# Kernel optimization log

Measured on AMD Instinct MI355X. Metric: run time of the kernel, lower is better.

## Reference

```python
import jax, jax.numpy as jnp
import numpy as np

B, N, C, DIM, K, E, NB = 16, 20000, 64, 128, 3, 640000, 3


def setup_inputs() -> dict:
    key = jax.random.key(0)
    ks = jax.random.split(key, 8)
    x = jax.random.normal(ks[0], (B, N * C), jnp.float32)
    edge_index = jax.random.randint(ks[1], (2, E), 0, N, jnp.int32)
    edge_weight = jax.random.uniform(ks[2], (E,), jnp.float32)
    # ChebConv: K Linear(C, dim, bias=False) weights + one shared bias per conv
    cheb_w = jax.random.normal(ks[3], (NB, K, C, DIM), jnp.float32) / np.float32(np.sqrt(C))
    cheb_b = jnp.zeros((NB, DIM), jnp.float32)
    beta = jnp.full((NB,), 0.5, jnp.float32)  # Swish beta, one shared act per block
    w1 = jax.random.normal(ks[4], (NB, DIM, DIM), jnp.float32) / np.float32(np.sqrt(DIM))
    b1 = jnp.zeros((NB, DIM), jnp.float32)
    w2 = jax.random.normal(ks[5], (NB, DIM, C), jnp.float32) / np.float32(np.sqrt(DIM))
    b2 = jnp.zeros((NB, C), jnp.float32)
    return dict(x=x, edge_index=edge_index, edge_weight=edge_weight,
                cheb_w=cheb_w, cheb_b=cheb_b, beta=beta, w1=w1, b1=b1, w2=w2, b2=b2)


def swish(x, beta):
    # (x * sigmoid(x * softplus(beta))) / 1.1
    return x * jax.nn.sigmoid(x * jax.nn.softplus(beta)) / 1.1


def reference(x, edge_index, edge_weight, cheb_w, cheb_b, beta, w1, b1, w2, b2):
    src, dst = edge_index[0], edge_index[1]
    # PyG ChebConv norm with lambda_max=2, sym: Lhat = L - I = -D^{-1/2} A D^{-1/2}
    deg = jax.ops.segment_sum(edge_weight, src, num_segments=N)
    dinv = jnp.where(deg > 0, jax.lax.rsqrt(jnp.maximum(deg, 1e-12)), 0.0)
    w = -dinv[src] * edge_weight * dinv[dst]  # [E]

    def spmm(h):  # h: [B, N, F] -> Lhat @ h per batch
        msg = h[:, src, :] * w[None, :, None]          # gather + scale, [B, E, F]
        return jnp.zeros_like(h).at[:, dst, :].add(msg)  # scatter-add

    h = x.reshape(B, N, C)
    for b in range(NB):  # fixed small layer loop
        # Chebyshev recurrence
        t0 = h
        t1 = spmm(t0)
        out = jnp.einsum('bnc,cd->bnd', t0, cheb_w[b, 0]) \
            + jnp.einsum('bnc,cd->bnd', t1, cheb_w[b, 1])
        tm2, tm1 = t0, t1
        for k in range(2, K):
            tk = 2.0 * spmm(tm1) - tm2
            out = out + jnp.einsum('bnc,cd->bnd', tk, cheb_w[b, k])
            tm2, tm1 = tm1, tk
        out = out + cheb_b[b]
        g = swish(out, beta[b])
        g = swish(g @ w1[b] + b1[b], beta[b])
        Fx = g @ w2[b] + b2[b]
        h = h + Fx  # invertible residual: output = Fx + x
    return h.reshape(B, N * C)
```

## Files before the change

### kernel.cpp

```cpp
#include <hip/hip_runtime.h>

namespace {
constexpr int   B_   = 16;
constexpr int   N_   = 20000;
constexpr int   C_   = 64;
constexpr int   DIM_ = 128;
constexpr int   E_   = 640000;
constexpr int   NB_  = 3;
constexpr int   ROW_ = B_ * C_;
constexpr int   NR_  = N_ * B_;

constexpr int   LDP  = 200;

constexpr int   PH_   = 16;
constexpr int   PCOL_ = ROW_ / PH_;
constexpr int   NPB_  = 16;
constexpr int   NCHK_ = N_ / NPB_;
constexpr int   NBIN_ = 1024;
constexpr int   NXCD_ = 8;
constexpr int   EP_   = E_ + 3 * N_ + 64;

constexpr int   SZ1_ = 128 * 192;
constexpr int   SZ2_ = 128 * 128;
constexpr int   SZ3_ = 64 * 128;
constexpr int   SZB_ = SZ1_ + SZ2_ + SZ3_;
constexpr int   WTOT_ = NB_ * SZB_;

constexpr size_t SZH_  = (size_t)N_ * ROW_ * sizeof(float);
constexpr size_t SZHB_ = (size_t)N_ * ROW_ * 2;
constexpr size_t OFF_H    = 0;
constexpr size_t OFF_HB   = SZH_;
constexpr size_t OFF_T1B  = OFF_HB  + SZHB_;
constexpr size_t OFF_SB   = OFF_T1B + SZHB_;
constexpr size_t OFF_DEG  = OFF_SB  + SZHB_;
constexpr size_t OFF_CNT  = OFF_DEG + (size_t)N_ * 4;
constexpr size_t OFF_OFFS = OFF_CNT + (size_t)N_ * 4;
constexpr size_t OFF_CV   = ((OFF_OFFS + (size_t)(N_ + 1) * 4 + 255) / 256) * 256;
constexpr size_t OFF_ESRC = OFF_CV;
constexpr size_t OFF_EW   = ((OFF_ESRC + (size_t)EP_ * 2 + 255) / 256) * 256;
static_assert(OFF_EW + (size_t)EP_ * 4 <= OFF_CV + (size_t)E_ * 8, "cv region overflow");
constexpr size_t OFF_PERM = OFF_CV   + (size_t)E_ * 8;
constexpr size_t OFF_HIST = OFF_PERM + (size_t)N_ * 4;
constexpr size_t OFF_HOFF = OFF_HIST + (size_t)NBIN_ * 4;
constexpr size_t OFF_HFIL = OFF_HOFF + (size_t)NBIN_ * 4;
constexpr size_t OFF_WTC  = OFF_HFIL + (size_t)NBIN_ * 4;
constexpr size_t OFF_WT1  = OFF_WTC + (size_t)NB_ * SZ1_ * 2;
constexpr size_t OFF_WT2  = OFF_WT1 + (size_t)NB_ * SZ2_ * 2;
}

typedef short s16x8 __attribute__((ext_vector_type(8)));
typedef float f32x4 __attribute__((ext_vector_type(4)));
typedef unsigned int u32;

__device__ __forceinline__ u32 bfr(float x) {
    u32 u = __float_as_uint(x);
    return (u + 0x7FFFu + ((u >> 16) & 1u)) >> 16;
}
__device__ __forceinline__ u32 pack_bf2(float x, float y) {
    return bfr(x) | (bfr(y) << 16);
}
__device__ __forceinline__ float bflo(u32 u) { return __uint_as_float(u << 16); }
__device__ __forceinline__ float bfhi(u32 u) { return __uint_as_float(u & 0xFFFF0000u); }

__global__ void deg_cnt_k(const int* __restrict__ src, const int* __restrict__ dst,
                          const float* __restrict__ ew,
                          float* __restrict__ deg, int* __restrict__ cnt) {
    int e = blockIdx.x * 256 + threadIdx.x;
    if (e < E_) {
        atomicAdd(deg + src[e], ew[e]);
        atomicAdd(cnt + dst[e], 1);
    }
}

__global__ void dinv_k(float* __restrict__ deg) {
    int i = blockIdx.x * 256 + threadIdx.x;
    if (i < N_) {
        float d = deg[i];
        deg[i] = (d > 0.f) ? rsqrtf(fmaxf(d, 1e-12f)) : 0.f;
    }
}

__global__ __launch_bounds__(1024) void scan_k(const int* __restrict__ cnt,
                                               int* __restrict__ offs) {
    __shared__ int sums[1024];
    const int tid = threadIdx.x;
    constexpr int CH = (N_ + 1023) / 1024;
    const int base = tid * CH;
    int local = 0;
    for (int j = 0; j < CH; ++j) {
        int i = base + j;
        if (i < N_) local += (cnt[i] + 3) & ~3;
    }
    sums[tid] = local;
    __syncthreads();
    for (int off = 1; off < 1024; off <<= 1) {
        int v = sums[tid];
        int u = (tid >= off) ? sums[tid - off] : 0;
        __syncthreads();
        sums[tid] = v + u;
        __syncthreads();
    }
    int run = (tid > 0) ? sums[tid - 1] : 0;
    for (int j = 0; j < CH; ++j) {
        int i = base + j;
        if (i < N_) { offs[i] = run; run += (cnt[i] + 3) & ~3; }
    }
    if (tid == 1023) offs[N_] = sums[1023];
}

__global__ void hist_k(const int* __restrict__ cnt, int* __restrict__ hist) {
    int i = blockIdx.x * 256 + threadIdx.x;
    if (i < N_) atomicAdd(hist + min(cnt[i], NBIN_ - 1), 1);
}

__global__ __launch_bounds__(1024) void hscan_k(const int* __restrict__ hist,
                                                int* __restrict__ hoffs) {
    __shared__ int s[NBIN_];
    int t = threadIdx.x;
    s[t] = hist[t];
    __syncthreads();
    for (int off = 1; off < NBIN_; off <<= 1) {
        int v = s[t];
        int u = (t >= off) ? s[t - off] : 0;
        __syncthreads();
        s[t] = v + u;
        __syncthreads();
    }
    hoffs[t] = (t > 0) ? s[t - 1] : 0;
}

__global__ void permscatter_k(const int* __restrict__ cnt, const int* __restrict__ hoffs,
                              int* __restrict__ hfill, int* __restrict__ perm) {
    int i = blockIdx.x * 256 + threadIdx.x;
    if (i < N_) {
        int b = min(cnt[i], NBIN_ - 1);
        int pos = hoffs[b] + atomicAdd(hfill + b, 1);
        perm[pos] = i;
    }
}

__global__ void scatter_k(const int* __restrict__ src, const int* __restrict__ dst,
                          const float* __restrict__ ew, const float* __restrict__ dinv,
                          const int* __restrict__ offs, int* __restrict__ fill,
                          ushort* __restrict__ esrc, float* __restrict__ eww) {
    int e = blockIdx.x * 256 + threadIdx.x;
    if (e < E_) {
        int s = src[e], d = dst[e];
        int pos = offs[d] + atomicAdd(fill + d, 1);
        float w = -dinv[s] * ew[e] * dinv[d];
        esrc[pos] = (ushort)s;
        eww[pos]  = w;
    }
}

__global__ void wprep_k(const float* __restrict__ cw, const float* __restrict__ w1,
                        const float* __restrict__ w2,
                        short* __restrict__ wtc, short* __restrict__ wt1,
                        short* __restrict__ wt2) {
    int idx = blockIdx.x * 256 + threadIdx.x;
    if (idx >= WTOT_) return;
    int b = idx / SZB_;
    int rem = idx - b * SZB_;
    if (rem < SZ1_) {
        int n = rem / 192, k = rem - n * 192;
        int part = k >> 6, c = k & 63;
        const float* base = cw + (size_t)b * 3 * 64 * 128;
        float v;
        if (part == 0)      v = base[c * 128 + n] - base[16384 + c * 128 + n];
        else if (part == 1) v = base[8192 + c * 128 + n];
        else                v = 2.f * base[16384 + c * 128 + n];
        wtc[(size_t)b * SZ1_ + n * 192 + k] = (short)bfr(v);
    } else if (rem < SZ1_ + SZ2_) {
        int r2 = rem - SZ1_;
        int n = r2 >> 7, k = r2 & 127;
        float v = w1[(size_t)b * 16384 + k * 128 + n];
        wt1[(size_t)b * SZ2_ + n * 128 + k] = (short)bfr(v);
    } else {
        int r3 = rem - SZ1_ - SZ2_;
        int n = r3 >> 7, k = r3 & 127;
        float v = w2[(size_t)b * 8192 + k * 64 + n];
        wt2[(size_t)b * SZ3_ + n * 128 + k] = (short)bfr(v);
    }
}

__global__ void transpose_in_k(const float* __restrict__ x, float* __restrict__ h,
                               ushort* __restrict__ hb) {
    int idx = blockIdx.x * 256 + threadIdx.x;
    int c4 = idx & 15;
    int nb = idx >> 4;
    int b  = nb & (B_ - 1);
    int n  = nb >> 4;
    const float4 v = *(const float4*)(x + ((size_t)b * N_ + n) * C_ + (c4 << 2));
    *(float4*)(h + (size_t)nb * C_ + (c4 << 2)) = v;
    uint2 p;
    p.x = pack_bf2(v.x, v.y);
    p.y = pack_bf2(v.z, v.w);
    *(uint2*)(hb + (size_t)nb * C_ + (c4 << 2)) = p;
}

__global__ void transpose_out_k(const float* __restrict__ h, float* __restrict__ out) {
    int idx = blockIdx.x * 256 + threadIdx.x;
    int c4 = idx & 15;
    int nb = idx >> 4;
    int b  = nb & (B_ - 1);
    int n  = nb >> 4;
    const float4 v = *(const float4*)(h + (size_t)nb * C_ + (c4 << 2));
    *(float4*)(out + ((size_t)b * N_ + n) * C_ + (c4 << 2)) = v;
}

__global__ __launch_bounds__(256) void spmm_ph_k(const ushort* __restrict__ in,
                                                 ushort* __restrict__ out,
                                                 const int* __restrict__ offs,
                                                 const ushort* __restrict__ esrc,
                                                 const float* __restrict__ eww,
                                                 const int* __restrict__ perm) {
    const int b    = blockIdx.x;
    const int xcd  = b & (NXCD_ - 1);
    const int slot = b >> 3;
    const int half = (slot >= NCHK_) ? 1 : 0;
    const int ph   = (xcd << 1) | half;
    const int chunk = slot - (half ? NCHK_ : 0);
    const int g      = threadIdx.x >> 4;
    const int lane16 = threadIdx.x & 15;
    const int n = perm[chunk * NPB_ + g];
    const int s0 = offs[n], s1 = offs[n + 1];
    const ushort* inp = in + (size_t)ph * PCOL_ + (lane16 << 2);

    float a0 = 0.f, a1 = 0.f, a2 = 0.f, a3 = 0.f;
    for (int i = s0; i < s1; i += 4) {
        ushort4 ss = *(const ushort4*)(esrc + i);
        float4  wf = *(const float4*)(eww + i);
        uint2 v0 = *(const uint2*)(inp + ((u32)ss.x << 10));
        uint2 v1 = *(const uint2*)(inp + ((u32)ss.y << 10));
        uint2 v2 = *(const uint2*)(inp + ((u32)ss.z << 10));
        uint2 v3 = *(const uint2*)(inp + ((u32)ss.w << 10));
        a0 += wf.x * bflo(v0.x) + wf.y * bflo(v1.x) + wf.z * bflo(v2.x) + wf.w * bflo(v3.x);
        a1 += wf.x * bfhi(v0.x) + wf.y * bfhi(v1.x) + wf.z * bfhi(v2.x) + wf.w * bfhi(v3.x);
        a2 += wf.x * bflo(v0.y) + wf.y * bflo(v1.y) + wf.z * bflo(v2.y) + wf.w * bflo(v3.y);
        a3 += wf.x * bfhi(v0.y) + wf.y * bfhi(v1.y) + wf.z * bfhi(v2.y) + wf.w * bfhi(v3.y);
    }
    uint2 p;
    p.x = pack_bf2(a0, a1);
    p.y = pack_bf2(a2, a3);
    *(uint2*)(out + (size_t)n * ROW_ + (size_t)ph * PCOL_ + (lane16 << 2)) = p;
}

__global__ __launch_bounds__(256, 4) void mlp_mfma_k(
        float* __restrict__ h, ushort* __restrict__ hb,
        const ushort* __restrict__ t1b, const ushort* __restrict__ sb,
        const short* __restrict__ wtc, const short* __restrict__ wt1,
        const short* __restrict__ wt2,
        const float* __restrict__ cbias, const float* __restrict__ b1,
        const float* __restrict__ b2, const float* __restrict__ betap) {
    __shared__ __align__(16) short u[64 * LDP];

    const int tid  = threadIdx.x;
    const int wv   = tid >> 6;
    const int lane = tid & 63;
    const int m    = lane & 15;
    const int q    = lane >> 4;
    const int row0 = blockIdx.x * 64;
    const float sp    = __logf(1.f + __expf(betap[0]));
    const float inv11 = 1.0f / 1.1f;

    s16x8 wA[6][2];
#pragma unroll
    for (int kb = 0; kb < 6; ++kb)
#pragma unroll
        for (int t = 0; t < 2; ++t)
            wA[kb][t] = *(const s16x8*)(wtc + ((wv << 5) + (t << 4) + m) * 192
                                            + (kb << 5) + (q << 3));

    {
        const ushort* srcs[3] = { hb, t1b, sb };
        s16x8 tv[3][2];
#pragma unroll
        for (int s = 0; s < 3; ++s)
#pragma unroll
            for (int i = 0; i < 2; ++i) {
                int ck = tid + (i << 8);
                int r = ck >> 3, c8 = ck & 7;
                tv[s][i] = *(const s16x8*)(srcs[s] + (size_t)(row0 + r) * C_ + (c8 << 3));
            }
#pragma unroll
        for (int s = 0; s < 3; ++s)
#pragma unroll
            for (int i = 0; i < 2; ++i) {
                int ck = tid + (i << 8);
                int r = ck >> 3, c8 = ck & 7;
                *(s16x8*)(u + r * LDP + (s << 6) + (c8 << 3)) = tv[s][i];
            }
    }
    __syncthreads();

    f32x4 acc[4][2];
#pragma unroll
    for (int rg = 0; rg < 4; ++rg)
#pragma unroll
        for (int t = 0; t < 2; ++t) acc[rg][t] = (f32x4){0.f, 0.f, 0.f, 0.f};
#pragma unroll
    for (int kb = 0; kb < 6; ++kb)
#pragma unroll
        for (int rg = 0; rg < 4; ++rg) {
            s16x8 af = *(const s16x8*)(u + ((rg << 4) + m) * LDP + (kb << 5) + (q << 3));
            acc[rg][0] = __builtin_amdgcn_mfma_f32_16x16x32_bf16(af, wA[kb][0], acc[rg][0], 0, 0, 0);
            acc[rg][1] = __builtin_amdgcn_mfma_f32_16x16x32_bf16(af, wA[kb][1], acc[rg][1], 0, 0, 0);
        }
    __syncthreads();

    s16x8 wB[4][2];
#pragma unroll
    for (int k4 = 0; k4 < 4; ++k4)
#pragma unroll
        for (int t = 0; t < 2; ++t)
            wB[k4][t] = *(const s16x8*)(wt1 + (((wv << 5) + (t << 4) + m) << 7)
                                            + (k4 << 5) + (q << 3));

    {
        float cb0 = cbias[(wv << 5) + m];
        float cb1 = cbias[(wv << 5) + 16 + m];
#pragma unroll
        for (int rg = 0; rg < 4; ++rg)
#pragma unroll
            for (int t = 0; t < 2; ++t) {
                float bv = t ? cb1 : cb0;
#pragma unroll
                for (int r = 0; r < 4; ++r) {
                    float o = acc[rg][t][r] + bv;
                    float g = o * (1.f / (1.f + __expf(-o * sp))) * inv11;
                    u[((rg << 4) + (q << 2) + r) * LDP + (wv << 5) + (t << 4) + m] =
                        (short)bfr(g);
                }
            }
    }
    __syncthreads();

    f32x4 acc2[4][2];
#pragma unroll
    for (int rg = 0; rg < 4; ++rg)
#pragma unroll
        for (int t = 0; t < 2; ++t) acc2[rg][t] = (f32x4){0.f, 0.f, 0.f, 0.f};
#pragma unroll
    for (int k4 = 0; k4 < 4; ++k4)
#pragma unroll
        for (int rg = 0; rg < 4; ++rg) {
            s16x8 af = *(const s16x8*)(u + ((rg << 4) + m) * LDP + (k4 << 5) + (q << 3));
            acc2[rg][0] = __builtin_amdgcn_mfma_f32_16x16x32_bf16(af, wB[k4][0], acc2[rg][0], 0, 0, 0);
            acc2[rg][1] = __builtin_amdgcn_mfma_f32_16x16x32_bf16(af, wB[k4][1], acc2[rg][1], 0, 0, 0);
        }
    __syncthreads();

    s16x8 wC[4];
#pragma unroll
    for (int k4 = 0; k4 < 4; ++k4)
        wC[k4] = *(const s16x8*)(wt2 + (((wv << 4) + m) << 7) + (k4 << 5) + (q << 3));

    {
        float b10 = b1[(wv << 5) + m];
        float b11 = b1[(wv << 5) + 16 + m];
#pragma unroll
        for (int rg = 0; rg < 4; ++rg)
#pragma unroll
            for (int t = 0; t < 2; ++t) {
                float bv = t ? b11 : b10;
#pragma unroll
                for (int r = 0; r < 4; ++r) {
                    float o = acc2[rg][t][r] + bv;
                    float g = o * (1.f / (1.f + __expf(-o * sp))) * inv11;
                    u[((rg << 4) + (q << 2) + r) * LDP + (wv << 5) + (t << 4) + m] =
                        (short)bfr(g);
                }
            }
    }
    __syncthreads();

    f32x4 acc3[4];
#pragma unroll
    for (int rg = 0; rg < 4; ++rg) acc3[rg] = (f32x4){0.f, 0.f, 0.f, 0.f};
#pragma unroll
    for (int k4 = 0; k4 < 4; ++k4)
#pragma unroll
        for (int rg = 0; rg < 4; ++rg) {
            s16x8 af = *(const s16x8*)(u + ((rg << 4) + m) * LDP + (k4 << 5) + (q << 3));
            acc3[rg] = __builtin_amdgcn_mfma_f32_16x16x32_bf16(af, wC[k4], acc3[rg], 0, 0, 0);
        }

    {
        float b2v = b2[(wv << 4) + m];
        float hv[4][4];
#pragma unroll
        for (int rg = 0; rg < 4; ++rg)
#pragma unroll
            for (int r = 0; r < 4; ++r)
                hv[rg][r] = h[(size_t)(row0 + (rg << 4) + (q << 2) + r) * C_
                              + (wv << 4) + m];
#pragma unroll
        for (int rg = 0; rg < 4; ++rg)
#pragma unroll
            for (int r = 0; r < 4; ++r) {
                size_t eidx = (size_t)(row0 + (rg << 4) + (q << 2) + r) * C_
                              + (wv << 4) + m;
                float nv = hv[rg][r] + acc3[rg][r] + b2v;
                h[eidx]  = nv;
                hb[eidx] = (ushort)bfr(nv);
            }
    }
}

extern "C" void kernel_launch(void* const* d_in, const int* in_sizes, int n_in,
                              void* d_out, int out_size, void* d_ws, size_t ws_size,
                              hipStream_t stream) {
    const float* x    = (const float*)d_in[0];
    const int*   ei   = (const int*)d_in[1];
    const float* ew   = (const float*)d_in[2];
    const float* cw   = (const float*)d_in[3];
    const float* cb   = (const float*)d_in[4];
    const float* beta = (const float*)d_in[5];
    const float* w1   = (const float*)d_in[6];
    const float* b1   = (const float*)d_in[7];
    const float* w2   = (const float*)d_in[8];
    const float* b2   = (const float*)d_in[9];
    float* out = (float*)d_out;

    char* ws = (char*)d_ws;
    float*  h_t  = (float*) (ws + OFF_H);
    ushort* hb   = (ushort*)(ws + OFF_HB);
    ushort* t1b  = (ushort*)(ws + OFF_T1B);
    ushort* sb   = (ushort*)(ws + OFF_SB);
    float*  deg  = (float*) (ws + OFF_DEG);
    int*    cnt  = (int*)   (ws + OFF_CNT);
    int*    offs = (int*)   (ws + OFF_OFFS);
    ushort* esrc = (ushort*)(ws + OFF_ESRC);
    float*  eww  = (float*) (ws + OFF_EW);
    int*    perm = (int*)   (ws + OFF_PERM);
    int*    hist = (int*)   (ws + OFF_HIST);
    int*    hoff = (int*)   (ws + OFF_HOFF);
    int*    hfil = (int*)   (ws + OFF_HFIL);
    short*  wtc  = (short*) (ws + OFF_WTC);
    short*  wt1  = (short*) (ws + OFF_WT1);
    short*  wt2  = (short*) (ws + OFF_WT2);

    const int* srcI = ei;
    const int* dstI = ei + E_;

    hipMemsetAsync(deg, 0, (size_t)N_ * 4, stream);
    hipMemsetAsync(cnt, 0, (size_t)N_ * 4, stream);
    hipMemsetAsync(hist, 0, (size_t)NBIN_ * 4, stream);
    hipMemsetAsync(hfil, 0, (size_t)NBIN_ * 4, stream);
    hipMemsetAsync(esrc, 0, (size_t)EP_ * 2, stream);
    hipMemsetAsync(eww,  0, (size_t)EP_ * 4, stream);
    deg_cnt_k<<<(E_ + 255) / 256, 256, 0, stream>>>(srcI, dstI, ew, deg, cnt);
    dinv_k<<<(N_ + 255) / 256, 256, 0, stream>>>(deg);
    scan_k<<<1, 1024, 0, stream>>>(cnt, offs);
    hist_k<<<(N_ + 255) / 256, 256, 0, stream>>>(cnt, hist);
    hscan_k<<<1, NBIN_, 0, stream>>>(hist, hoff);
    permscatter_k<<<(N_ + 255) / 256, 256, 0, stream>>>(cnt, hoff, hfil, perm);
    hipMemsetAsync(cnt, 0, (size_t)N_ * 4, stream);
    scatter_k<<<(E_ + 255) / 256, 256, 0, stream>>>(srcI, dstI, ew, deg, offs, cnt,
                                                    esrc, eww);

    wprep_k<<<(WTOT_ + 255) / 256, 256, 0, stream>>>(cw, w1, w2, wtc, wt1, wt2);

    transpose_in_k<<<(N_ * B_ * 16) / 256, 256, 0, stream>>>(x, h_t, hb);

    for (int b = 0; b < NB_; ++b) {
        spmm_ph_k<<<PH_ * NCHK_, 256, 0, stream>>>(hb, t1b, offs, esrc, eww, perm);
        spmm_ph_k<<<PH_ * NCHK_, 256, 0, stream>>>(t1b, sb, offs, esrc, eww, perm);
        mlp_mfma_k<<<NR_ / 64, 256, 0, stream>>>(h_t, hb, t1b, sb,
                                                 wtc + (size_t)b * SZ1_,
                                                 wt1 + (size_t)b * SZ2_,
                                                 wt2 + (size_t)b * SZ3_,
                                                 cb + (size_t)b * DIM_,
                                                 b1 + (size_t)b * DIM_,
                                                 b2 + (size_t)b * C_,
                                                 beta + b);
    }

    transpose_out_k<<<(N_ * B_ * 16) / 256, 256, 0, stream>>>(h_t, out);
}
```

Measured before the change: 1.404 ms.

## Widen SpMM gathers to 16 bytes, drop XCD column split, prefetch edge indices

```diff
diff --git a/kernel.cpp b/kernel.cpp
--- a/kernel.cpp
+++ b/kernel.cpp
@@ -12,12 +12,11 @@
 
 constexpr int   LDP  = 200;
 
-constexpr int   PH_   = 16;
-constexpr int   PCOL_ = ROW_ / PH_;
+constexpr int   SPH_  = 8;
+constexpr int   PC2_  = ROW_ / SPH_;
 constexpr int   NPB_  = 16;
 constexpr int   NCHK_ = N_ / NPB_;
 constexpr int   NBIN_ = 1024;
-constexpr int   NXCD_ = 8;
 constexpr int   EP_   = E_ + 3 * N_ + 64;
 
 constexpr int   SZ1_ = 128 * 192;
@@ -50,7 +49,12 @@
 
 typedef short s16x8 __attribute__((ext_vector_type(8)));
 typedef float f32x4 __attribute__((ext_vector_type(4)));
+typedef float f32x2 __attribute__((ext_vector_type(2)));
 typedef unsigned int u32;
+typedef u32   u32x4 __attribute__((ext_vector_type(4)));
+typedef u32   u32x2 __attribute__((ext_vector_type(2)));
+typedef unsigned short u16;
+typedef u16   u16x4 __attribute__((ext_vector_type(4)));
 
 __device__ __forceinline__ u32 bfr(float x) {
     u32 u = __float_as_uint(x);
@@ -59,8 +63,12 @@
 __device__ __forceinline__ u32 pack_bf2(float x, float y) {
     return bfr(x) | (bfr(y) << 16);
 }
-__device__ __forceinline__ float bflo(u32 u) { return __uint_as_float(u << 16); }
-__device__ __forceinline__ float bfhi(u32 u) { return __uint_as_float(u & 0xFFFF0000u); }
+__device__ __forceinline__ f32x2 bfpair(u32 u) {
+    u32x2 r;
+    r.x = u << 16;
+    r.y = u & 0xFFFF0000u;
+    return __builtin_bit_cast(f32x2, r);
+}
 
 __global__ void deg_cnt_k(const int* __restrict__ src, const int* __restrict__ dst,
                           const float* __restrict__ ew,
@@ -214,35 +222,54 @@
                                                  const ushort* __restrict__ esrc,
                                                  const float* __restrict__ eww,
                                                  const int* __restrict__ perm) {
-    const int b    = blockIdx.x;
-    const int xcd  = b & (NXCD_ - 1);
-    const int slot = b >> 3;
-    const int half = (slot >= NCHK_) ? 1 : 0;
-    const int ph   = (xcd << 1) | half;
-    const int chunk = slot - (half ? NCHK_ : 0);
+    const int b     = blockIdx.x;
+    const int sph   = b & (SPH_ - 1);
+    const int chunk = b >> 3;
     const int g      = threadIdx.x >> 4;
     const int lane16 = threadIdx.x & 15;
     const int n = perm[chunk * NPB_ + g];
     const int s0 = offs[n], s1 = offs[n + 1];
-    const ushort* inp = in + (size_t)ph * PCOL_ + (lane16 << 2);
-
-    float a0 = 0.f, a1 = 0.f, a2 = 0.f, a3 = 0.f;
-    for (int i = s0; i < s1; i += 4) {
-        ushort4 ss = *(const ushort4*)(esrc + i);
-        float4  wf = *(const float4*)(eww + i);
-        uint2 v0 = *(const uint2*)(inp + ((u32)ss.x << 10));
-        uint2 v1 = *(const uint2*)(inp + ((u32)ss.y << 10));
-        uint2 v2 = *(const uint2*)(inp + ((u32)ss.z << 10));
-        uint2 v3 = *(const uint2*)(inp + ((u32)ss.w << 10));
-        a0 += wf.x * bflo(v0.x) + wf.y * bflo(v1.x) + wf.z * bflo(v2.x) + wf.w * bflo(v3.x);
-        a1 += wf.x * bfhi(v0.x) + wf.y * bfhi(v1.x) + wf.z * bfhi(v2.x) + wf.w * bfhi(v3.x);
-        a2 += wf.x * bflo(v0.y) + wf.y * bflo(v1.y) + wf.z * bflo(v2.y) + wf.w * bflo(v3.y);
-        a3 += wf.x * bfhi(v0.y) + wf.y * bfhi(v1.y) + wf.z * bfhi(v2.y) + wf.w * bfhi(v3.y);
-    }
-    uint2 p;
-    p.x = pack_bf2(a0, a1);
-    p.y = pack_bf2(a2, a3);
-    *(uint2*)(out + (size_t)n * ROW_ + (size_t)ph * PCOL_ + (lane16 << 2)) = p;
+    const ushort* inp = in + (size_t)sph * PC2_ + (lane16 << 3);
+
+    f32x2 a0 = {0.f, 0.f}, a1 = {0.f, 0.f}, a2 = {0.f, 0.f}, a3 = {0.f, 0.f};
+    if (s0 < s1) {
+        u16x4 sCur = *(const u16x4*)(esrc + s0);
+        f32x4 wCur = *(const f32x4*)(eww + s0);
+        u16x4 sMid = *(const u16x4*)(esrc + s0 + 4);
+        f32x4 wMid = *(const f32x4*)(eww + s0 + 4);
+        for (int i = s0; i < s1; i += 4) {
+            u32x4 v0 = *(const u32x4*)(inp + ((u32)sCur.x << 10));
+            u32x4 v1 = *(const u32x4*)(inp + ((u32)sCur.y << 10));
+            u32x4 v2 = *(const u32x4*)(inp + ((u32)sCur.z << 10));
+            u32x4 v3 = *(const u32x4*)(inp + ((u32)sCur.w << 10));
+            u16x4 sFar = *(const u16x4*)(esrc + i + 8);
+            f32x4 wFar = *(const f32x4*)(eww + i + 8);
+            a0 += (f32x2){wCur.x, wCur.x} * bfpair(v0.x);
+            a1 += (f32x2){wCur.x, wCur.x} * bfpair(v0.y);
+            a2 += (f32x2){wCur.x, wCur.x} * bfpair(v0.z);
+            a3 += (f32x2){wCur.x, wCur.x} * bfpair(v0.w);
+            a0 += (f32x2){wCur.y, wCur.y} * bfpair(v1.x);
+            a1 += (f32x2){wCur.y, wCur.y} * bfpair(v1.y);
+            a2 += (f32x2){wCur.y, wCur.y} * bfpair(v1.z);
+            a3 += (f32x2){wCur.y, wCur.y} * bfpair(v1.w);
+            a0 += (f32x2){wCur.z, wCur.z} * bfpair(v2.x);
+            a1 += (f32x2){wCur.z, wCur.z} * bfpair(v2.y);
+            a2 += (f32x2){wCur.z, wCur.z} * bfpair(v2.z);
+            a3 += (f32x2){wCur.z, wCur.z} * bfpair(v2.w);
+            a0 += (f32x2){wCur.w, wCur.w} * bfpair(v3.x);
+            a1 += (f32x2){wCur.w, wCur.w} * bfpair(v3.y);
+            a2 += (f32x2){wCur.w, wCur.w} * bfpair(v3.z);
+            a3 += (f32x2){wCur.w, wCur.w} * bfpair(v3.w);
+            sCur = sMid; wCur = wMid;
+            sMid = sFar; wMid = wFar;
+        }
+    }
+    u32x4 p;
+    p.x = pack_bf2(a0.x, a0.y);
+    p.y = pack_bf2(a1.x, a1.y);
+    p.z = pack_bf2(a2.x, a2.y);
+    p.w = pack_bf2(a3.x, a3.y);
+    *(u32x4*)(out + (size_t)n * ROW_ + (size_t)sph * PC2_ + (lane16 << 3)) = p;
 }
 
 __global__ __launch_bounds__(256, 4) void mlp_mfma_k(
@@ -464,8 +491,8 @@
     transpose_in_k<<<(N_ * B_ * 16) / 256, 256, 0, stream>>>(x, h_t, hb);
 
     for (int b = 0; b < NB_; ++b) {
-        spmm_ph_k<<<PH_ * NCHK_, 256, 0, stream>>>(hb, t1b, offs, esrc, eww, perm);
-        spmm_ph_k<<<PH_ * NCHK_, 256, 0, stream>>>(t1b, sb, offs, esrc, eww, perm);
+        spmm_ph_k<<<SPH_ * NCHK_, 256, 0, stream>>>(hb, t1b, offs, esrc, eww, perm);
+        spmm_ph_k<<<SPH_ * NCHK_, 256, 0, stream>>>(t1b, sb, offs, esrc, eww, perm);
         mlp_mfma_k<<<NR_ / 64, 256, 0, stream>>>(h_t, hb, t1b, sb,
                                                  wtc + (size_t)b * SZ1_,
                                                  wt1 + (size_t)b * SZ2_,
```

Result: faster. 1.276 ms (-9.1%).

## Widen SpMM gathers to 16-byte loads, pad rows to 8, prefetch indices

Applied to the files above, without the earlier changes.

```diff
diff --git a/kernel.cpp b/kernel.cpp
--- a/kernel.cpp
+++ b/kernel.cpp
@@ -14,11 +14,11 @@
 
 constexpr int   PH_   = 16;
 constexpr int   PCOL_ = ROW_ / PH_;
-constexpr int   NPB_  = 16;
+constexpr int   NPB_  = 32;
 constexpr int   NCHK_ = N_ / NPB_;
 constexpr int   NBIN_ = 1024;
 constexpr int   NXCD_ = 8;
-constexpr int   EP_   = E_ + 3 * N_ + 64;
+constexpr int   EP_   = E_ + 7 * N_ + 64;
 
 constexpr int   SZ1_ = 128 * 192;
 constexpr int   SZ2_ = 128 * 128;
@@ -50,7 +50,12 @@
 
 typedef short s16x8 __attribute__((ext_vector_type(8)));
 typedef float f32x4 __attribute__((ext_vector_type(4)));
+typedef float f32x2 __attribute__((ext_vector_type(2)));
 typedef unsigned int u32;
+typedef u32   u32x4 __attribute__((ext_vector_type(4)));
+typedef u32   u32x2 __attribute__((ext_vector_type(2)));
+typedef unsigned short u16;
+typedef u16   u16x8 __attribute__((ext_vector_type(8)));
 
 __device__ __forceinline__ u32 bfr(float x) {
     u32 u = __float_as_uint(x);
@@ -59,8 +64,12 @@
 __device__ __forceinline__ u32 pack_bf2(float x, float y) {
     return bfr(x) | (bfr(y) << 16);
 }
-__device__ __forceinline__ float bflo(u32 u) { return __uint_as_float(u << 16); }
-__device__ __forceinline__ float bfhi(u32 u) { return __uint_as_float(u & 0xFFFF0000u); }
+__device__ __forceinline__ f32x2 bfpair(u32 u) {
+    u32x2 r;
+    r.x = u << 16;
+    r.y = u & 0xFFFF0000u;
+    return __builtin_bit_cast(f32x2, r);
+}
 
 __global__ void deg_cnt_k(const int* __restrict__ src, const int* __restrict__ dst,
                           const float* __restrict__ ew,
@@ -89,7 +98,7 @@
     int local = 0;
     for (int j = 0; j < CH; ++j) {
         int i = base + j;
-        if (i < N_) local += (cnt[i] + 3) & ~3;
+        if (i < N_) local += (cnt[i] + 7) & ~7;
     }
     sums[tid] = local;
     __syncthreads();
@@ -103,7 +112,7 @@
     int run = (tid > 0) ? sums[tid - 1] : 0;
     for (int j = 0; j < CH; ++j) {
         int i = base + j;
-        if (i < N_) { offs[i] = run; run += (cnt[i] + 3) & ~3; }
+        if (i < N_) { offs[i] = run; run += (cnt[i] + 7) & ~7; }
     }
     if (tid == 1023) offs[N_] = sums[1023];
 }
@@ -214,35 +223,80 @@
                                                  const ushort* __restrict__ esrc,
                                                  const float* __restrict__ eww,
                                                  const int* __restrict__ perm) {
-    const int b    = blockIdx.x;
-    const int xcd  = b & (NXCD_ - 1);
-    const int slot = b >> 3;
-    const int half = (slot >= NCHK_) ? 1 : 0;
-    const int ph   = (xcd << 1) | half;
+    const int b     = blockIdx.x;
+    const int xcd   = b & (NXCD_ - 1);
+    const int slot  = b >> 3;
+    const int half  = (slot >= NCHK_) ? 1 : 0;
+    const int ph    = (xcd << 1) | half;
     const int chunk = slot - (half ? NCHK_ : 0);
-    const int g      = threadIdx.x >> 4;
-    const int lane16 = threadIdx.x & 15;
+    const int g     = threadIdx.x >> 3;
+    const int lane8 = threadIdx.x & 7;
     const int n = perm[chunk * NPB_ + g];
     const int s0 = offs[n], s1 = offs[n + 1];
-    const ushort* inp = in + (size_t)ph * PCOL_ + (lane16 << 2);
-
-    float a0 = 0.f, a1 = 0.f, a2 = 0.f, a3 = 0.f;
-    for (int i = s0; i < s1; i += 4) {
-        ushort4 ss = *(const ushort4*)(esrc + i);
-        float4  wf = *(const float4*)(eww + i);
-        uint2 v0 = *(const uint2*)(inp + ((u32)ss.x << 10));
-        uint2 v1 = *(const uint2*)(inp + ((u32)ss.y << 10));
-        uint2 v2 = *(const uint2*)(inp + ((u32)ss.z << 10));
-        uint2 v3 = *(const uint2*)(inp + ((u32)ss.w << 10));
-        a0 += wf.x * bflo(v0.x) + wf.y * bflo(v1.x) + wf.z * bflo(v2.x) + wf.w * bflo(v3.x);
-        a1 += wf.x * bfhi(v0.x) + wf.y * bfhi(v1.x) + wf.z * bfhi(v2.x) + wf.w * bfhi(v3.x);
-        a2 += wf.x * bflo(v0.y) + wf.y * bflo(v1.y) + wf.z * bflo(v2.y) + wf.w * bflo(v3.y);
-        a3 += wf.x * bfhi(v0.y) + wf.y * bfhi(v1.y) + wf.z * bfhi(v2.y) + wf.w * bfhi(v3.y);
-    }
-    uint2 p;
-    p.x = pack_bf2(a0, a1);
-    p.y = pack_bf2(a2, a3);
-    *(uint2*)(out + (size_t)n * ROW_ + (size_t)ph * PCOL_ + (lane16 << 2)) = p;
+    const ushort* inp = in + (size_t)ph * PCOL_ + (lane8 << 3);
+
+    f32x2 a0 = {0.f, 0.f}, a1 = {0.f, 0.f}, a2 = {0.f, 0.f}, a3 = {0.f, 0.f};
+    if (s0 < s1) {
+        u16x8 sCur = *(const u16x8*)(esrc + s0);
+        f32x4 wCurA = *(const f32x4*)(eww + s0);
+        f32x4 wCurB = *(const f32x4*)(eww + s0 + 4);
+        u16x8 sMid = *(const u16x8*)(esrc + s0 + 8);
+        f32x4 wMidA = *(const f32x4*)(eww + s0 + 8);
+        f32x4 wMidB = *(const f32x4*)(eww + s0 + 12);
+        for (int i = s0; i < s1; i += 8) {
+            u32x4 v0 = *(const u32x4*)(inp + ((u32)sCur[0] << 10));
+            u32x4 v1 = *(const u32x4*)(inp + ((u32)sCur[1] << 10));
+            u32x4 v2 = *(const u32x4*)(inp + ((u32)sCur[2] << 10));
+            u32x4 v3 = *(const u32x4*)(inp + ((u32)sCur[3] << 10));
+            u32x4 v4 = *(const u32x4*)(inp + ((u32)sCur[4] << 10));
+            u32x4 v5 = *(const u32x4*)(inp + ((u32)sCur[5] << 10));
+            u32x4 v6 = *(const u32x4*)(inp + ((u32)sCur[6] << 10));
+            u32x4 v7 = *(const u32x4*)(inp + ((u32)sCur[7] << 10));
+            u16x8 sFar = *(const u16x8*)(esrc + i + 16);
+            f32x4 wFarA = *(const f32x4*)(eww + i + 16);
+            f32x4 wFarB = *(const f32x4*)(eww + i + 20);
+            a0 += (f32x2){wCurA.x, wCurA.x} * bfpair(v0.x);
+            a1 += (f32x2){wCurA.x, wCurA.x} * bfpair(v0.y);
+            a2 += (f32x2){wCurA.x, wCurA.x} * bfpair(v0.z);
+            a3 += (f32x2){wCurA.x, wCurA.x} * bfpair(v0.w);
+            a0 += (f32x2){wCurA.y, wCurA.y} * bfpair(v1.x);
+            a1 += (f32x2){wCurA.y, wCurA.y} * bfpair(v1.y);
+            a2 += (f32x2){wCurA.y, wCurA.y} * bfpair(v1.z);
+            a3 += (f32x2){wCurA.y, wCurA.y} * bfpair(v1.w);
+            a0 += (f32x2){wCurA.z, wCurA.z} * bfpair(v2.x);
+            a1 += (f32x2){wCurA.z, wCurA.z} * bfpair(v2.y);
+            a2 += (f32x2){wCurA.z, wCurA.z} * bfpair(v2.z);
+            a3 += (f32x2){wCurA.z, wCurA.z} * bfpair(v2.w);
+            a0 += (f32x2){wCurA.w, wCurA.w} * bfpair(v3.x);
+            a1 += (f32x2){wCurA.w, wCurA.w} * bfpair(v3.y);
+            a2 += (f32x2){wCurA.w, wCurA.w} * bfpair(v3.z);
+            a3 += (f32x2){wCurA.w, wCurA.w} * bfpair(v3.w);
+            a0 += (f32x2){wCurB.x, wCurB.x} * bfpair(v4.x);
+            a1 += (f32x2){wCurB.x, wCurB.x} * bfpair(v4.y);
+            a2 += (f32x2){wCurB.x, wCurB.x} * bfpair(v4.z);
+            a3 += (f32x2){wCurB.x, wCurB.x} * bfpair(v4.w);
+            a0 += (f32x2){wCurB.y, wCurB.y} * bfpair(v5.x);
+            a1 += (f32x2){wCurB.y, wCurB.y} * bfpair(v5.y);
+            a2 += (f32x2){wCurB.y, wCurB.y} * bfpair(v5.z);
+            a3 += (f32x2){wCurB.y, wCurB.y} * bfpair(v5.w);
+            a0 += (f32x2){wCurB.z, wCurB.z} * bfpair(v6.x);
+            a1 += (f32x2){wCurB.z, wCurB.z} * bfpair(v6.y);
+            a2 += (f32x2){wCurB.z, wCurB.z} * bfpair(v6.z);
+            a3 += (f32x2){wCurB.z, wCurB.z} * bfpair(v6.w);
+            a0 += (f32x2){wCurB.w, wCurB.w} * bfpair(v7.x);
+            a1 += (f32x2){wCurB.w, wCurB.w} * bfpair(v7.y);
+            a2 += (f32x2){wCurB.w, wCurB.w} * bfpair(v7.z);
+            a3 += (f32x2){wCurB.w, wCurB.w} * bfpair(v7.w);
+            sCur = sMid; wCurA = wMidA; wCurB = wMidB;
+            sMid = sFar; wMidA = wFarA; wMidB = wFarB;
+        }
+    }
+    u32x4 p;
+    p.x = pack_bf2(a0.x, a0.y);
+    p.y = pack_bf2(a1.x, a1.y);
+    p.z = pack_bf2(a2.x, a2.y);
+    p.w = pack_bf2(a3.x, a3.y);
+    *(u32x4*)(out + (size_t)n * ROW_ + (size_t)ph * PCOL_ + (lane8 << 3)) = p;
 }
 
 __global__ __launch_bounds__(256, 4) void mlp_mfma_k(
```

Result: faster. 1.174 ms (-16.4%).
